# Performance work log

Hardware: AMD Instinct MI355X
Metric: run time of the kernel (lower is better)

Reference implementation:

```python
import jax, jax.numpy as jnp
import numpy as np

N = 50000       # nodes
E = 800000      # edges (before self-loops)
IN_DIM = 128
HID = 16
H1 = 8
OUT_DIM = 16
H2 = 1
NEG_SLOPE = 0.2  # PyG GATConv LeakyReLU negative slope


def setup_inputs() -> dict:
    key = jax.random.key(0)
    ks = jax.random.split(key, 10)
    x = jax.random.normal(ks[0], (N, IN_DIM), dtype=jnp.float32)
    edge_index = jax.random.randint(ks[1], (2, E), 0, N, dtype=jnp.int32)
    # layer 1: Linear(IN_DIM -> H1*HID, no bias), att vectors [H, C], bias [H1*HID]
    W1 = jax.random.normal(ks[2], (IN_DIM, H1 * HID), dtype=jnp.float32) / np.sqrt(IN_DIM).astype(np.float32)
    a_src1 = jax.random.normal(ks[3], (H1, HID), dtype=jnp.float32) * 0.1
    a_dst1 = jax.random.normal(ks[4], (H1, HID), dtype=jnp.float32) * 0.1
    b1 = jnp.zeros((H1 * HID,), dtype=jnp.float32)
    # layer 2: Linear(H1*HID -> H2*OUT_DIM), concat=False -> bias [OUT_DIM]
    W2 = jax.random.normal(ks[5], (H1 * HID, H2 * OUT_DIM), dtype=jnp.float32) / np.sqrt(H1 * HID).astype(np.float32)
    a_src2 = jax.random.normal(ks[6], (H2, OUT_DIM), dtype=jnp.float32) * 0.1
    a_dst2 = jax.random.normal(ks[7], (H2, OUT_DIM), dtype=jnp.float32) * 0.1
    b2 = jnp.zeros((OUT_DIM,), dtype=jnp.float32)
    return {"x": x, "edge_index": edge_index, "W1": W1, "a_src1": a_src1,
            "a_dst1": a_dst1, "b1": b1, "W2": W2, "a_src2": a_src2,
            "a_dst2": a_dst2, "b2": b2}


def gat_conv(x, src, dst, W, a_src, a_dst, bias, heads, ch, concat):
    n = x.shape[0]
    h = (x @ W).reshape(n, heads, ch)                      # [N,H,C]
    s_src = jnp.sum(h * a_src, axis=-1)                    # [N,H] att_src . Wx
    s_dst = jnp.sum(h * a_dst, axis=-1)                    # [N,H]
    e = jax.nn.leaky_relu(s_src[src] + s_dst[dst], NEG_SLOPE)  # [Etot,H]
    # segment softmax over incoming edges per target node
    m = jax.ops.segment_max(e, dst, num_segments=n)        # [N,H]
    ee = jnp.exp(e - m[dst])
    denom = jax.ops.segment_sum(ee, dst, num_segments=n)   # [N,H]
    alpha = ee / denom[dst]                                # [Etot,H]
    out = jax.ops.segment_sum(h[src] * alpha[:, :, None], dst, num_segments=n)  # [N,H,C]
    out = out.reshape(n, heads * ch) if concat else out.mean(axis=1)
    return out + bias


def reference(x, edge_index, W1, a_src1, a_dst1, b1, W2, a_src2, a_dst2, b2):
    n = x.shape[0]
    loop = jnp.arange(n, dtype=edge_index.dtype)           # PyG adds self-loops
    src = jnp.concatenate([edge_index[0], loop])
    dst = jnp.concatenate([edge_index[1], loop])
    # eval mode: F.dropout is identity
    h = jax.nn.elu(gat_conv(x, src, dst, W1, a_src1, a_dst1, b1, H1, HID, True))
    out = gat_conv(h, src, dst, W2, a_src2, a_dst2, b2, H2, OUT_DIM, False)
    return jax.nn.log_softmax(out, axis=1)
```

## Files before the change

kernel.cpp:

```cpp
#include <hip/hip_runtime.h>
#include <hip/hip_fp16.h>
#include <math.h>

#define NEG_SLOPE 0.2f
#define MAXDEG 64

typedef short bf16x8 __attribute__((ext_vector_type(8)));
typedef float f32x4 __attribute__((ext_vector_type(4)));

__device__ __forceinline__ unsigned short f2bf(float f) {
    union { float f; unsigned u; } v; v.f = f;
    unsigned r = v.u + 0x7FFF + ((v.u >> 16) & 1);
    return (unsigned short)(r >> 16);
}

__global__ void k_init(const float* __restrict__ W1, unsigned short* __restrict__ Wt,
                       int* __restrict__ cursor, int N)
{
    int gid = blockIdx.x * 256 + threadIdx.x;
    if (gid < 16384) {
        int col = gid >> 7, k = gid & 127;
        Wt[col * 128 + k] = f2bf(W1[k * 128 + col]);
    }
    if (gid < N) cursor[gid] = 0;
}

__global__ __launch_bounds__(256) void k_mega(
    const float* __restrict__ x, const unsigned short* __restrict__ Wt,
    const float* __restrict__ a_src, const float* __restrict__ a_dst,
    __half* __restrict__ h1h, float* __restrict__ ssrc, float* __restrict__ sdst,
    int N, int G1,
    const int* __restrict__ src_e, const int* __restrict__ dst_e, int E,
    int* __restrict__ cursor, unsigned short* __restrict__ csr)
{
    __shared__ unsigned short ws[128 * 128];
    const int t = threadIdx.x;

    if (blockIdx.x >= G1) {
        int i = (blockIdx.x - G1) * 256 + t;
        int Etot = E + N;
        if (i >= Etot) return;
        int s, d;
        if (i < E) { s = src_e[i]; d = dst_e[i]; } else { s = d = i - E; }
        int pos = atomicAdd(&cursor[d], 1);
        if (pos < MAXDEG) csr[d * MAXDEG + pos] = (unsigned short)s;
        return;
    }

    const int r0 = blockIdx.x * 64;
    for (int ch = t; ch < 2048; ch += 256) {
        int col = ch >> 4;
        int k8 = ch & 15;
        bf16x8 v = *(const bf16x8*)(Wt + col * 128 + k8 * 8);
        int addr = (col * 256 + k8 * 16) ^ ((col & 7) << 4);
        *(bf16x8*)((char*)ws + addr) = v;
    }
    __syncthreads();

    const int w = t >> 6, l = t & 63;
    const int lo = l & 15, hi = l >> 4;
    const int row = r0 + w * 16 + lo;
    const bool rok = (row < N);

    f32x4 acc[8] = {};
    #pragma unroll
    for (int kk = 0; kk < 4; ++kk) {
        bf16x8 a;
        {
            float4 f0 = make_float4(0.f,0.f,0.f,0.f), f1 = f0;
            if (rok) {
                const float4* xp = (const float4*)(x + (size_t)row * 128 + kk * 32 + hi * 8);
                f0 = xp[0]; f1 = xp[1];
            }
            a[0] = (short)f2bf(f0.x); a[1] = (short)f2bf(f0.y);
            a[2] = (short)f2bf(f0.z); a[3] = (short)f2bf(f0.w);
            a[4] = (short)f2bf(f1.x); a[5] = (short)f2bf(f1.y);
            a[6] = (short)f2bf(f1.z); a[7] = (short)f2bf(f1.w);
        }
        #pragma unroll
        for (int c = 0; c < 8; ++c) {
            int col = c * 16 + lo;
            int addr = (col * 256 + kk * 64 + hi * 16) ^ ((col & 7) << 4);
            bf16x8 b = *(const bf16x8*)((char*)ws + addr);
            acc[c] = __builtin_amdgcn_mfma_f32_16x16x32_bf16(a, b, acc[c], 0, 0, 0);
        }
    }

    float av_s[8], av_d[8];
    #pragma unroll
    for (int c = 0; c < 8; ++c) {
        av_s[c] = a_src[c * 16 + lo];
        av_d[c] = a_dst[c * 16 + lo];
    }

    #pragma unroll
    for (int reg = 0; reg < 4; ++reg) {
        int grow = r0 + w * 16 + hi * 4 + reg;
        bool ok = (grow < N);
        if (ok) {
            #pragma unroll
            for (int c = 0; c < 8; ++c)
                h1h[(size_t)grow * 128 + c * 16 + lo] = __float2half(acc[c][reg]);
        }
        #pragma unroll
        for (int c = 0; c < 8; ++c) {
            float ps = acc[c][reg] * av_s[c];
            float pd = acc[c][reg] * av_d[c];
            #pragma unroll
            for (int m = 8; m >= 1; m >>= 1) {
                ps += __shfl_xor(ps, m, 64);
                pd += __shfl_xor(pd, m, 64);
            }
            if (ok && lo == 0) {
                ssrc[grow * 8 + c] = ps;
                sdst[grow * 8 + c] = pd;
            }
        }
    }
}

__global__ __launch_bounds__(256) void k_aggr1g2(
    const int* __restrict__ deg, const unsigned short* __restrict__ csr,
    const __half2* __restrict__ h1h, const float* __restrict__ ssrc,
    const float* __restrict__ sdst, const float* __restrict__ b1,
    const float* __restrict__ W2, const float* __restrict__ a_src2,
    const float* __restrict__ a_dst2,
    float* __restrict__ h2, float* __restrict__ s2s, float* __restrict__ s2d, int N)
{
    __shared__ float lds_w2[2048];
    __shared__ float lds_h[4][128];
    const int t = threadIdx.x;

    {
        const float4* src = (const float4*)W2;
        float4* dst = (float4*)lds_w2;
        #pragma unroll
        for (int i = 0; i < 2; ++i) dst[i * 256 + t] = src[i * 256 + t];
    }
    __syncthreads();

    const int wid = t >> 6;
    const int lane = t & 63;
    const int node = blockIdx.x * 4 + wid;
    if (node >= N) return;
    const int h = lane >> 3;
    const int beg = node * MAXDEG;
    const int end = beg + min(deg[node], MAXDEG);
    const float sd = sdst[node * 8 + h];
    float acc0 = 0.f, acc1 = 0.f, wsum = 0.f;

    int j = beg;
    for (; j + 3 < end; j += 4) {
        int s0 = csr[j], s1 = csr[j + 1], s2 = csr[j + 2], s3 = csr[j + 3];
        float e0 = ssrc[s0 * 8 + h];
        float e1 = ssrc[s1 * 8 + h];
        float e2 = ssrc[s2 * 8 + h];
        float e3 = ssrc[s3 * 8 + h];
        __half2 v0 = h1h[(size_t)s0 * 64 + lane];
        __half2 v1 = h1h[(size_t)s1 * 64 + lane];
        __half2 v2 = h1h[(size_t)s2 * 64 + lane];
        __half2 v3 = h1h[(size_t)s3 * 64 + lane];
        e0 += sd; e0 = (e0 >= 0.f) ? e0 : NEG_SLOPE * e0; float w0 = __expf(e0);
        e1 += sd; e1 = (e1 >= 0.f) ? e1 : NEG_SLOPE * e1; float w1 = __expf(e1);
        e2 += sd; e2 = (e2 >= 0.f) ? e2 : NEG_SLOPE * e2; float w2 = __expf(e2);
        e3 += sd; e3 = (e3 >= 0.f) ? e3 : NEG_SLOPE * e3; float w3 = __expf(e3);
        wsum += (w0 + w1) + (w2 + w3);
        float2 f0 = __half22float2(v0);
        float2 f1 = __half22float2(v1);
        float2 f2 = __half22float2(v2);
        float2 f3 = __half22float2(v3);
        acc0 = fmaf(w0, f0.x, acc0); acc1 = fmaf(w0, f0.y, acc1);
        acc0 = fmaf(w1, f1.x, acc0); acc1 = fmaf(w1, f1.y, acc1);
        acc0 = fmaf(w2, f2.x, acc0); acc1 = fmaf(w2, f2.y, acc1);
        acc0 = fmaf(w3, f3.x, acc0); acc1 = fmaf(w3, f3.y, acc1);
    }
    for (; j < end; ++j) {
        int s = csr[j];
        float e = ssrc[s * 8 + h] + sd;
        e = (e >= 0.f) ? e : NEG_SLOPE * e;
        float w = __expf(e);
        wsum += w;
        float2 f = __half22float2(h1h[(size_t)s * 64 + lane]);
        acc0 = fmaf(w, f.x, acc0); acc1 = fmaf(w, f.y, acc1);
    }

    const float2 bb = ((const float2*)b1)[lane];
    float inv = 1.f / wsum;
    float va = acc0 * inv + bb.x;
    float vb = acc1 * inv + bb.y;
    va = (va > 0.f) ? va : expm1f(va);
    vb = (vb > 0.f) ? vb : expm1f(vb);

    lds_h[wid][2 * lane]     = va;
    lds_h[wid][2 * lane + 1] = vb;
    asm volatile("s_waitcnt lgkmcnt(0)" ::: "memory");

    const int col = lane & 15, kg = lane >> 4;
    float r = 0.f;
    #pragma unroll
    for (int k2 = 0; k2 < 32; ++k2) {
        int k = kg * 32 + k2;
        r = fmaf(lds_h[wid][k], lds_w2[k * 16 + col], r);
    }
    r += __shfl_xor(r, 16, 64);
    r += __shfl_xor(r, 32, 64);
    if (lane < 16) h2[(size_t)node * 16 + col] = r;

    float ps = r * a_src2[col];
    float pd = r * a_dst2[col];
    #pragma unroll
    for (int m = 8; m >= 1; m >>= 1) {
        ps += __shfl_xor(ps, m, 64);
        pd += __shfl_xor(pd, m, 64);
    }
    if (lane == 0) { s2s[node] = ps; s2d[node] = pd; }
}

__global__ __launch_bounds__(256) void k_aggr2(
    const int* __restrict__ deg, const unsigned short* __restrict__ csr,
    const float* __restrict__ h2, const float* __restrict__ s2s,
    const float* __restrict__ s2d, const float* __restrict__ b2,
    float* __restrict__ out, int N)
{
    int gid = blockIdx.x * 256 + threadIdx.x;
    int node = gid >> 4;
    if (node >= N) return;
    int c = gid & 15;
    const int beg = node * MAXDEG;
    const int end = beg + min(deg[node], MAXDEG);
    float sd = s2d[node];
    float acc = 0.f, wsum = 0.f;

    int j = beg;
    for (; j + 3 < end; j += 4) {
        int s0 = csr[j], s1 = csr[j + 1], s2 = csr[j + 2], s3 = csr[j + 3];
        float e0 = s2s[s0], e1 = s2s[s1], e2 = s2s[s2], e3 = s2s[s3];
        float g0 = h2[(size_t)s0 * 16 + c];
        float g1 = h2[(size_t)s1 * 16 + c];
        float g2 = h2[(size_t)s2 * 16 + c];
        float g3 = h2[(size_t)s3 * 16 + c];
        e0 += sd; e0 = (e0 >= 0.f) ? e0 : NEG_SLOPE * e0; float w0 = __expf(e0);
        e1 += sd; e1 = (e1 >= 0.f) ? e1 : NEG_SLOPE * e1; float w1 = __expf(e1);
        e2 += sd; e2 = (e2 >= 0.f) ? e2 : NEG_SLOPE * e2; float w2 = __expf(e2);
        e3 += sd; e3 = (e3 >= 0.f) ? e3 : NEG_SLOPE * e3; float w3 = __expf(e3);
        wsum += (w0 + w1) + (w2 + w3);
        acc = fmaf(w0, g0, acc);
        acc = fmaf(w1, g1, acc);
        acc = fmaf(w2, g2, acc);
        acc = fmaf(w3, g3, acc);
    }
    for (; j < end; ++j) {
        int s = csr[j];
        float e = s2s[s] + sd;
        e = (e >= 0.f) ? e : NEG_SLOPE * e;
        float w = __expf(e);
        wsum += w;
        acc = fmaf(w, h2[(size_t)s * 16 + c], acc);
    }

    float v = acc / wsum + b2[c];
    float m = v;
    #pragma unroll
    for (int msk = 8; msk >= 1; msk >>= 1) m = fmaxf(m, __shfl_xor(m, msk, 64));
    float ex = __expf(v - m);
    float sum = ex;
    #pragma unroll
    for (int msk = 8; msk >= 1; msk >>= 1) sum += __shfl_xor(sum, msk, 64);
    out[(size_t)node * 16 + c] = v - m - __logf(sum);
}

extern "C" void kernel_launch(void* const* d_in, const int* in_sizes, int n_in,
                              void* d_out, int out_size, void* d_ws, size_t ws_size,
                              hipStream_t stream)
{
    const float* x      = (const float*)d_in[0];
    const int*   ei     = (const int*)  d_in[1];
    const float* W1     = (const float*)d_in[2];
    const float* a_src1 = (const float*)d_in[3];
    const float* a_dst1 = (const float*)d_in[4];
    const float* b1     = (const float*)d_in[5];
    const float* W2     = (const float*)d_in[6];
    const float* a_src2 = (const float*)d_in[7];
    const float* a_dst2 = (const float*)d_in[8];
    const float* b2     = (const float*)d_in[9];
    float* out = (float*)d_out;

    const int N = in_sizes[0] / 128;
    const int E = in_sizes[1] / 2;
    const int Etot = E + N;
    const int* src_e = ei;
    const int* dst_e = ei + E;

    float* p = (float*)d_ws;
    __half* h1h  = (__half*)p; p += (size_t)N * 64;
    unsigned short* Wt = (unsigned short*)p; p += 8192;
    float* ssrc1 = p; p += (size_t)N * 8;
    float* sdst1 = p; p += (size_t)N * 8;
    float* h2    = p; p += (size_t)N * 16;
    float* s2s   = p; p += (size_t)N;
    float* s2d   = p; p += (size_t)N;
    int* ip = (int*)p;
    int* cursor = ip; ip += N;
    unsigned short* csr = (unsigned short*)ip;

    const int G1 = (N + 63) / 64;
    const int GF = (Etot + 255) / 256;

    k_init<<<(N + 255) / 256, 256, 0, stream>>>(W1, Wt, cursor, N);

    k_mega<<<G1 + GF, 256, 0, stream>>>(
        x, Wt, a_src1, a_dst1, h1h, ssrc1, sdst1, N, G1,
        src_e, dst_e, E, cursor, csr);

    k_aggr1g2<<<(N + 3) / 4, 256, 0, stream>>>(
        cursor, csr, (const __half2*)h1h, ssrc1, sdst1, b1,
        W2, a_src2, a_dst2, h2, s2s, s2d, N);

    k_aggr2<<<((size_t)N * 16 + 255) / 256, 256, 0, stream>>>(
        cursor, csr, h2, s2s, s2d, b2, out, N);
}
```

Baseline: 144.0 us.

## Pre-swizzle W1 into MFMA fragments, pad degree counters, seed self-loops in init

```diff
diff --git a/kernel.cpp b/kernel.cpp
--- a/kernel.cpp
+++ b/kernel.cpp
@@ -4,6 +4,7 @@
 
 #define NEG_SLOPE 0.2f
 #define MAXDEG 64
+#define CSTRIDE 16
 
 typedef short bf16x8 __attribute__((ext_vector_type(8)));
 typedef float f32x4 __attribute__((ext_vector_type(4)));
@@ -14,49 +15,43 @@
     return (unsigned short)(r >> 16);
 }
 
-__global__ void k_init(const float* __restrict__ W1, unsigned short* __restrict__ Wt,
-                       int* __restrict__ cursor, int N)
+__global__ void k_init(const float* __restrict__ W1, unsigned short* __restrict__ frag,
+                       int* __restrict__ cursor, unsigned short* __restrict__ csr, int N)
 {
     int gid = blockIdx.x * 256 + threadIdx.x;
     if (gid < 16384) {
-        int col = gid >> 7, k = gid & 127;
-        Wt[col * 128 + k] = f2bf(W1[k * 128 + col]);
-    }
-    if (gid < N) cursor[gid] = 0;
+        int f = gid >> 3, j = gid & 7;
+        int kk = f >> 9, c = (f >> 6) & 7, l = f & 63;
+        int col = c * 16 + (l & 15);
+        int k = kk * 32 + ((l >> 4) << 3) + j;
+        frag[gid] = f2bf(W1[k * 128 + col]);
+    }
+    if (gid < N) {
+        cursor[gid * CSTRIDE] = 1;
+        csr[gid * MAXDEG] = (unsigned short)gid;
+    }
 }
 
 __global__ __launch_bounds__(256) void k_mega(
-    const float* __restrict__ x, const unsigned short* __restrict__ Wt,
+    const float* __restrict__ x, const bf16x8* __restrict__ frag,
     const float* __restrict__ a_src, const float* __restrict__ a_dst,
     __half* __restrict__ h1h, float* __restrict__ ssrc, float* __restrict__ sdst,
     int N, int G1,
     const int* __restrict__ src_e, const int* __restrict__ dst_e, int E,
     int* __restrict__ cursor, unsigned short* __restrict__ csr)
 {
-    __shared__ unsigned short ws[128 * 128];
     const int t = threadIdx.x;
 
     if (blockIdx.x >= G1) {
         int i = (blockIdx.x - G1) * 256 + t;
-        int Etot = E + N;
-        if (i >= Etot) return;
-        int s, d;
-        if (i < E) { s = src_e[i]; d = dst_e[i]; } else { s = d = i - E; }
-        int pos = atomicAdd(&cursor[d], 1);
+        if (i >= E) return;
+        int s = src_e[i], d = dst_e[i];
+        int pos = atomicAdd(&cursor[d * CSTRIDE], 1);
         if (pos < MAXDEG) csr[d * MAXDEG + pos] = (unsigned short)s;
         return;
     }
 
     const int r0 = blockIdx.x * 64;
-    for (int ch = t; ch < 2048; ch += 256) {
-        int col = ch >> 4;
-        int k8 = ch & 15;
-        bf16x8 v = *(const bf16x8*)(Wt + col * 128 + k8 * 8);
-        int addr = (col * 256 + k8 * 16) ^ ((col & 7) << 4);
-        *(bf16x8*)((char*)ws + addr) = v;
-    }
-    __syncthreads();
-
     const int w = t >> 6, l = t & 63;
     const int lo = l & 15, hi = l >> 4;
     const int row = r0 + w * 16 + lo;
@@ -79,9 +74,7 @@
         }
         #pragma unroll
         for (int c = 0; c < 8; ++c) {
-            int col = c * 16 + lo;
-            int addr = (col * 256 + kk * 64 + hi * 16) ^ ((col & 7) << 4);
-            bf16x8 b = *(const bf16x8*)((char*)ws + addr);
+            bf16x8 b = frag[(kk * 8 + c) * 64 + l];
             acc[c] = __builtin_amdgcn_mfma_f32_16x16x32_bf16(a, b, acc[c], 0, 0, 0);
         }
     }
@@ -120,7 +113,7 @@
 }
 
 __global__ __launch_bounds__(256) void k_aggr1g2(
-    const int* __restrict__ deg, const unsigned short* __restrict__ csr,
+    const int* __restrict__ cursor, const unsigned short* __restrict__ csr,
     const __half2* __restrict__ h1h, const float* __restrict__ ssrc,
     const float* __restrict__ sdst, const float* __restrict__ b1,
     const float* __restrict__ W2, const float* __restrict__ a_src2,
@@ -145,7 +138,7 @@
     if (node >= N) return;
     const int h = lane >> 3;
     const int beg = node * MAXDEG;
-    const int end = beg + min(deg[node], MAXDEG);
+    const int end = beg + min(cursor[node * CSTRIDE], MAXDEG);
     const float sd = sdst[node * 8 + h];
     float acc0 = 0.f, acc1 = 0.f, wsum = 0.f;
 
@@ -217,7 +210,7 @@
 }
 
 __global__ __launch_bounds__(256) void k_aggr2(
-    const int* __restrict__ deg, const unsigned short* __restrict__ csr,
+    const int* __restrict__ cursor, const unsigned short* __restrict__ csr,
     const float* __restrict__ h2, const float* __restrict__ s2s,
     const float* __restrict__ s2d, const float* __restrict__ b2,
     float* __restrict__ out, int N)
@@ -227,7 +220,7 @@
     if (node >= N) return;
     int c = gid & 15;
     const int beg = node * MAXDEG;
-    const int end = beg + min(deg[node], MAXDEG);
+    const int end = beg + min(cursor[node * CSTRIDE], MAXDEG);
     float sd = s2d[node];
     float acc = 0.f, wsum = 0.f;
 
@@ -287,29 +280,28 @@
 
     const int N = in_sizes[0] / 128;
     const int E = in_sizes[1] / 2;
-    const int Etot = E + N;
     const int* src_e = ei;
     const int* dst_e = ei + E;
 
     float* p = (float*)d_ws;
     __half* h1h  = (__half*)p; p += (size_t)N * 64;
-    unsigned short* Wt = (unsigned short*)p; p += 8192;
+    unsigned short* frag = (unsigned short*)p; p += 8192;
     float* ssrc1 = p; p += (size_t)N * 8;
     float* sdst1 = p; p += (size_t)N * 8;
     float* h2    = p; p += (size_t)N * 16;
     float* s2s   = p; p += (size_t)N;
     float* s2d   = p; p += (size_t)N;
     int* ip = (int*)p;
-    int* cursor = ip; ip += N;
+    int* cursor = ip; ip += (size_t)N * CSTRIDE;
     unsigned short* csr = (unsigned short*)ip;
 
     const int G1 = (N + 63) / 64;
-    const int GF = (Etot + 255) / 256;
-
-    k_init<<<(N + 255) / 256, 256, 0, stream>>>(W1, Wt, cursor, N);
+    const int GF = (E + 255) / 256;
+
+    k_init<<<(N + 255) / 256, 256, 0, stream>>>(W1, frag, cursor, csr, N);
 
     k_mega<<<G1 + GF, 256, 0, stream>>>(
-        x, Wt, a_src1, a_dst1, h1h, ssrc1, sdst1, N, G1,
+        x, (const bf16x8*)frag, a_src1, a_dst1, h1h, ssrc1, sdst1, N, G1,
         src_e, dst_e, E, cursor, csr);
 
     k_aggr1g2<<<(N + 3) / 4, 256, 0, stream>>>(
```

New measurement: 132.2 us. -8.2%, faster.
